# Kernel optimization log

Hardware: AMD Instinct MI355X
Metric: run time of the kernel (lower is better)

The kernel has to match this reference:

```python
import jax, jax.numpy as jnp
import numpy as np

N_NODES = 100000
N_EDGES = 3200000
BN_EPS = 1e-5


def setup_inputs() -> dict:
    key = jax.random.key(0)
    ks = jax.random.split(key, 16)
    return {
        "x": jax.random.normal(ks[0], (N_NODES, 2), jnp.float32),
        "eq_labels": jax.random.randint(ks[1], (N_NODES,), 0, 32, jnp.int32),
        "edge_index": jax.random.randint(ks[2], (2, N_EDGES), 0, N_NODES, jnp.int32),
        "eq_emb": jax.random.normal(ks[3], (32, 8), jnp.float32),
        "W1_0": jax.random.normal(ks[4], (10, 64), jnp.float32) * 0.3,
        "b1_0": jnp.zeros((64,), jnp.float32),
        "W2_0": jax.random.normal(ks[5], (64, 64), jnp.float32) * 0.12,
        "b2_0": jnp.zeros((64,), jnp.float32),
        "eps_0": jnp.zeros((), jnp.float32),
        "gamma_0": jnp.ones((64,), jnp.float32),
        "beta_0": jnp.zeros((64,), jnp.float32),
        "W1_s": jax.random.normal(ks[6], (2, 64, 64), jnp.float32) * 0.12,
        "b1_s": jnp.zeros((2, 64), jnp.float32),
        "W2_s": jax.random.normal(ks[7], (2, 64, 64), jnp.float32) * 0.12,
        "b2_s": jnp.zeros((2, 64), jnp.float32),
        "eps_s": jnp.zeros((2,), jnp.float32),
        "gamma_s": jnp.ones((2, 64), jnp.float32),
        "beta_s": jnp.zeros((2, 64), jnp.float32),
        "Wf": jax.random.normal(ks[8], (64, 1), jnp.float32) * 0.12,
        "bf": jnp.zeros((1,), jnp.float32),
    }


def _gin_bn_relu(h, src, dst, W1, b1, W2, b2, eps, gamma, beta):
    # GINConv: (1+eps)*x_i + sum_{j->i} x_j, then 2-layer ReLU MLP, then BN, ReLU
    agg = jax.ops.segment_sum(h[src], dst, num_segments=N_NODES)
    h = (1.0 + eps) * h + agg
    h = jax.nn.relu(h @ W1 + b1)
    h = jax.nn.relu(h @ W2 + b2)
    mu = jnp.mean(h, axis=0)
    var = jnp.var(h, axis=0)
    h = (h - mu) * jax.lax.rsqrt(var + BN_EPS) * gamma + beta
    return jax.nn.relu(h)


def reference(x, eq_labels, edge_index, eq_emb, W1_0, b1_0, W2_0, b2_0, eps_0,
              gamma_0, beta_0, W1_s, b1_s, W2_s, b2_s, eps_s, gamma_s, beta_s,
              Wf, bf):
    src, dst = edge_index[0], edge_index[1]
    h = jnp.concatenate([x, eq_emb[eq_labels]], axis=-1)  # [N, 10]
    h = _gin_bn_relu(h, src, dst, W1_0, b1_0, W2_0, b2_0, eps_0, gamma_0, beta_0)
    for i in range(2):
        h = _gin_bn_relu(h, src, dst, W1_s[i], b1_s[i], W2_s[i], b2_s[i],
                         eps_s[i], gamma_s[i], beta_s[i])
    return (h @ Wf + bf).squeeze(-1)  # [N]
```

## Files before the change

kernel.cpp:

```cpp
#include <hip/hip_runtime.h>

#define N_NODES 100000
#define N_EDGES 3200000
#define BN_EPS 1e-5f

#define BLK_NODES 128
#define NBLK 782
#define CHUNK 16384
#define NW ((N_EDGES + CHUNK - 1) / CHUNK)
#define BCAP 4480
#define CUR_PAD 16
#define NSLICE 32

typedef unsigned int uint;
typedef unsigned short ushort;
typedef _Float16 half_t;
typedef __attribute__((ext_vector_type(8))) _Float16 h8v;
typedef __attribute__((ext_vector_type(4))) float f4v;

__device__ inline float bf_lo(uint u) { return __uint_as_float(u << 16); }
__device__ inline float bf_hi(uint u) { return __uint_as_float(u & 0xffff0000u); }
__device__ inline float h_lo(uint u) {
    union { ushort s; half_t h; } r; r.s = (ushort)(u & 0xffffu); return (float)r.h;
}
__device__ inline float h_hi(uint u) {
    union { ushort s; half_t h; } r; r.s = (ushort)(u >> 16); return (float)r.h;
}
__device__ inline ushort f2bf(float a) {
    uint ua = __float_as_uint(a); ua += 0x7fffu + ((ua >> 16) & 1u);
    return (ushort)(ua >> 16);
}
__device__ inline ushort f2h(float a) {
    union { half_t h; ushort u; } r;
    r.h = (half_t)a;
    return r.u;
}
__device__ inline uint packh2(float a, float b) {
    return (uint)f2h(a) | ((uint)f2h(b) << 16);
}
__device__ inline h8v loadH(const ushort* p) {
    union { uint4 q; h8v f; } r;
    r.q = *(const uint4*)p;
    return r.f;
}
__device__ inline h8v loadHh(const half_t* p) {
    union { uint4 q; h8v f; } r;
    r.q = *(const uint4*)p;
    return r.f;
}
__device__ inline f4v mfma16(h8v a, h8v b, f4v c) {
    return __builtin_amdgcn_mfma_f32_16x16x32_f16(a, b, c, 0, 0, 0);
}

__global__ __launch_bounds__(256) void k_h0(const float* __restrict__ x,
                                            const int* __restrict__ lab,
                                            const float* __restrict__ emb,
                                            ushort* __restrict__ h0,
                                            const float* __restrict__ W1_0,
                                            const float* __restrict__ W2_0,
                                            const float* __restrict__ W1_s,
                                            const float* __restrict__ W2_s,
                                            ushort* __restrict__ W0t,
                                            ushort* __restrict__ W20t,
                                            ushort* __restrict__ Wst, int n) {
    int i = blockIdx.x * blockDim.x + threadIdx.x;
    if (i < n) {
        float v[16];
        v[0] = x[2 * i];
        v[1] = x[2 * i + 1];
        int L = lab[i];
#pragma unroll
        for (int k = 0; k < 8; k++) v[2 + k] = emb[L * 8 + k];
#pragma unroll
        for (int k = 10; k < 16; k++) v[k] = 0.f;
        uint o8[8];
#pragma unroll
        for (int k = 0; k < 8; k++) o8[k] = packh2(v[2 * k], v[2 * k + 1]);
        uint4* o = (uint4*)(h0 + (size_t)i * 16);
        o[0] = uint4{o8[0], o8[1], o8[2], o8[3]};
        o[1] = uint4{o8[4], o8[5], o8[6], o8[7]};
    }
    if (blockIdx.x == 0) {
        int t = threadIdx.x;
        for (int j = t; j < 64 * 32; j += 256) {
            int nn = j >> 5, k = j & 31;
            W0t[j] = (k < 10) ? f2h(W1_0[k * 64 + nn]) : (ushort)0;
        }
        for (int j = t; j < 4096; j += 256) {
            int nn = j >> 6, k = j & 63;
            W20t[j] = f2h(W2_0[k * 64 + nn]);
        }
        for (int l = 0; l < 2; l++) {
            const float* w1 = W1_s + l * 4096;
            const float* w2 = W2_s + l * 4096;
            for (int j = t; j < 4096; j += 256) {
                int nn = j >> 6, k = j & 63;
                Wst[l * 8192 + j] = f2h(w1[k * 64 + nn]);
                Wst[l * 8192 + 4096 + j] = f2h(w2[k * 64 + nn]);
            }
        }
    }
}

__global__ __launch_bounds__(256) void k_fill(const int* __restrict__ src,
                                              const int* __restrict__ dst,
                                              int* __restrict__ gcur,
                                              int* __restrict__ bucket) {
    __shared__ int cnt[NBLK];
    __shared__ int off[NBLK];
    int t = threadIdx.x;
    for (int b = t; b < NBLK; b += 256) cnt[b] = 0;
    __syncthreads();
    int my0 = blockIdx.x * CHUNK + t * 64;
    for (int k = 0; k < 64; k += 4) {
        int e = my0 + k;
        if (e + 3 < N_EDGES) {
            int4 d4 = *(const int4*)(dst + e);
            atomicAdd(&cnt[d4.x >> 7], 1);
            atomicAdd(&cnt[d4.y >> 7], 1);
            atomicAdd(&cnt[d4.z >> 7], 1);
            atomicAdd(&cnt[d4.w >> 7], 1);
        } else {
#pragma unroll
            for (int kk = 0; kk < 4; kk++) {
                int ee = e + kk;
                if (ee < N_EDGES) atomicAdd(&cnt[dst[ee] >> 7], 1);
            }
        }
    }
    __syncthreads();
    for (int b = t; b < NBLK; b += 256) {
        int c = cnt[b];
        off[b] = (c > 0) ? atomicAdd(&gcur[b * CUR_PAD], c) : 0;
    }
    __syncthreads();
    for (int k = 0; k < 64; k += 4) {
        int e = my0 + k;
        if (e + 3 < N_EDGES) {
            int4 d4 = *(const int4*)(dst + e);
            int4 s4 = *(const int4*)(src + e);
            int dd[4] = {d4.x, d4.y, d4.z, d4.w};
            int ss[4] = {s4.x, s4.y, s4.z, s4.w};
#pragma unroll
            for (int kk = 0; kk < 4; kk++) {
                int b = dd[kk] >> 7;
                int p = atomicAdd(&off[b], 1);
                if (p < BCAP)
                    bucket[(size_t)b * BCAP + p] = ((dd[kk] & 127) << 17) | ss[kk];
            }
        } else {
#pragma unroll
            for (int kk = 0; kk < 4; kk++) {
                int ee = e + kk;
                if (ee < N_EDGES) {
                    int d = dst[ee], s = src[ee];
                    int b = d >> 7;
                    int p = atomicAdd(&off[b], 1);
                    if (p < BCAP)
                        bucket[(size_t)b * BCAP + p] = ((d & 127) << 17) | s;
                }
            }
        }
    }
}

__global__ __launch_bounds__(256) void k_sort(const int* __restrict__ gcur,
                                              const int* __restrict__ bucket,
                                              int* __restrict__ col2,
                                              int2* __restrict__ nodeoff, int n) {
    __shared__ int cnt[BLK_NODES];
    __shared__ int scn[BLK_NODES];
    __shared__ int cur[BLK_NODES];
    int t = threadIdx.x;
    int blk = blockIdx.x;
    if (t < BLK_NODES) cnt[t] = 0;
    __syncthreads();
    int cc = min(gcur[blk * CUR_PAD], BCAP);
    const int* bb = bucket + (size_t)blk * BCAP;
    for (int i = t; i < cc; i += 256) atomicAdd(&cnt[bb[i] >> 17], 1);
    __syncthreads();
    if (t < BLK_NODES) scn[t] = cnt[t];
    __syncthreads();
#pragma unroll
    for (int off = 1; off < BLK_NODES; off <<= 1) {
        int v = (t >= off && t < BLK_NODES) ? scn[t - off] : 0;
        __syncthreads();
        if (t < BLK_NODES) scn[t] += v;
        __syncthreads();
    }
    if (t < BLK_NODES) {
        int start = scn[t] - cnt[t];
        cur[t] = start;
        int node = blk * BLK_NODES + t;
        if (node < n) nodeoff[node] = int2{blk * BCAP + start, cnt[t]};
    }
    __syncthreads();
    int* out = col2 + (size_t)blk * BCAP;
    for (int i = t; i < cc; i += 256) {
        int w = bb[i];
        int p = atomicAdd(&cur[w >> 17], 1);
        out[p] = w & 0x1FFFF;
    }
}

__global__ __launch_bounds__(256, 4) void k_layer0M(const ushort* __restrict__ h0,
                                                    const int2* __restrict__ nodeoff,
                                                    const int* __restrict__ col,
                                                    const float* __restrict__ epsp,
                                                    const ushort* __restrict__ W0t,
                                                    const float* __restrict__ b1,
                                                    const ushort* __restrict__ W20t,
                                                    const float* __restrict__ b2,
                                                    ushort* __restrict__ hraw,
                                                    float* __restrict__ part_out) {
    __shared__ half_t buf[4][16][72];
    int t = threadIdx.x, w = t >> 6, lane = t & 63;
    int base = blockIdx.x * 64 + w * 16;
    float ep = 1.f + *epsp;
    int hl = lane >> 5, l5 = lane & 31;
    int q = l5 & 3, g = l5 >> 2;
    const uint* hb = (const uint*)h0;

    int nj = base + (lane & 15);
    int2 no2 = nodeoff[nj];
    int myStart = no2.x;
    int myDeg = (nj < N_NODES) ? no2.y : 0;

    int stC, dgC, mxC, wvC, wv2C;
    {
        stC = __shfl(myStart, hl, 64);
        dgC = __shfl(myDeg, hl, 64);
        int dA = __shfl(myDeg, 0, 64), dB = __shfl(myDeg, 1, 64);
        mxC = max(dA, dB);
        wvC = (dgC > 0) ? col[stC + min(l5, dgC - 1)] : 0;
        wv2C = (mxC > 32) ? ((dgC > 32) ? col[stC + min(32 + l5, dgC - 1)] : wvC) : 0;
    }

    for (int r = 0; r < 8; r++) {
        int stN = 0, dgN = 0, mxN = 0, wvN = 0, wv2N = 0;
        if (r < 7) {
            stN = __shfl(myStart, 2 * (r + 1) + hl, 64);
            dgN = __shfl(myDeg, 2 * (r + 1) + hl, 64);
            int dA = __shfl(myDeg, 2 * (r + 1), 64);
            int dB = __shfl(myDeg, 2 * (r + 1) + 1, 64);
            mxN = max(dA, dB);
            wvN = (dgN > 0) ? col[stN + min(l5, dgN - 1)] : 0;
            wv2N = (mxN > 32) ? ((dgN > 32) ? col[stN + min(32 + l5, dgN - 1)] : wvN) : 0;
        }
        int deg = dgC, mx = mxC;
        float ac[4] = {0.f, 0.f, 0.f, 0.f};
        if (mx > 0) {
            int idx[4];
#pragma unroll
            for (int i = 0; i < 4; i++) idx[i] = __shfl(wvC, (hl << 5) + g + 8 * i, 64);
            uint2 rows[4];
#pragma unroll
            for (int i = 0; i < 4; i++)
                rows[i] = *(const uint2*)(hb + (size_t)idx[i] * 8 + q * 2);
#pragma unroll
            for (int i = 0; i < 4; i++) {
                float m = (g + 8 * i < deg) ? 1.f : 0.f;
                ac[0] = fmaf(m, h_lo(rows[i].x), ac[0]);
                ac[1] = fmaf(m, h_hi(rows[i].x), ac[1]);
                ac[2] = fmaf(m, h_lo(rows[i].y), ac[2]);
                ac[3] = fmaf(m, h_hi(rows[i].y), ac[3]);
            }
            if (mx > 32) {
                int idx2[4];
#pragma unroll
                for (int i = 0; i < 4; i++) idx2[i] = __shfl(wv2C, (hl << 5) + g + 8 * i, 64);
                uint2 rows2[4];
#pragma unroll
                for (int i = 0; i < 4; i++)
                    rows2[i] = *(const uint2*)(hb + (size_t)idx2[i] * 8 + q * 2);
#pragma unroll
                for (int i = 0; i < 4; i++) {
                    float m = (32 + g + 8 * i < deg) ? 1.f : 0.f;
                    ac[0] = fmaf(m, h_lo(rows2[i].x), ac[0]);
                    ac[1] = fmaf(m, h_hi(rows2[i].x), ac[1]);
                    ac[2] = fmaf(m, h_lo(rows2[i].y), ac[2]);
                    ac[3] = fmaf(m, h_hi(rows2[i].y), ac[3]);
                }
                for (int e = 64 + g; e < deg; e += 8) {
                    uint2 v = *(const uint2*)(hb + (size_t)col[stC + e] * 8 + q * 2);
                    ac[0] += h_lo(v.x); ac[1] += h_hi(v.x);
                    ac[2] += h_lo(v.y); ac[3] += h_hi(v.y);
                }
            }
        }
#pragma unroll
        for (int o = 4; o < 32; o <<= 1) {
#pragma unroll
            for (int k = 0; k < 4; k++) ac[k] += __shfl_xor(ac[k], o, 64);
        }
        int node = base + 2 * r + hl;
        bool valid = node < N_NODES;
        int nodeC = valid ? node : 0;
        float vm = valid ? ep : 0.f;
        uint2 sv = *(const uint2*)(hb + (size_t)nodeC * 8 + q * 2);
        ac[0] = fmaf(vm, h_lo(sv.x), ac[0]);
        ac[1] = fmaf(vm, h_hi(sv.x), ac[1]);
        ac[2] = fmaf(vm, h_lo(sv.y), ac[2]);
        ac[3] = fmaf(vm, h_hi(sv.y), ac[3]);
        if (!valid) { ac[0] = ac[1] = ac[2] = ac[3] = 0.f; }
        if (g == 0) {
            int nl = 2 * r + hl;
            *(uint2*)&buf[w][nl][q * 4] = uint2{packh2(ac[0], ac[1]), packh2(ac[2], ac[3])};
            *(uint2*)&buf[w][nl][16 + q * 4] = uint2{0u, 0u};
        }
        stC = stN; dgC = dgN; mxC = mxN; wvC = wvN; wv2C = wv2N;
    }
    int mr = lane & 15, kq = lane >> 4, nc = lane & 15;
    h8v A0 = loadHh(&buf[w][mr][kq * 8]);
#pragma unroll
    for (int nt = 0; nt < 4; nt++) {
        float bb = b1[nt * 16 + nc];
        f4v c = {bb, bb, bb, bb};
        c = mfma16(A0, loadH(W0t + (nt * 16 + nc) * 32 + kq * 8), c);
#pragma unroll
        for (int r2 = 0; r2 < 4; r2++)
            buf[w][kq * 4 + r2][nt * 16 + nc] = (half_t)fmaxf(c[r2], 0.f);
    }
    h8v P0 = loadHh(&buf[w][mr][kq * 8]);
    h8v P1 = loadHh(&buf[w][mr][32 + kq * 8]);
    float sA[4], sB[4];
#pragma unroll
    for (int nt = 0; nt < 4; nt++) { sA[nt] = 0.f; sB[nt] = 0.f; }
#pragma unroll
    for (int nt = 0; nt < 4; nt++) {
        float bb = b2[nt * 16 + nc];
        f4v c = {bb, bb, bb, bb};
        c = mfma16(P0, loadH(W20t + (nt * 16 + nc) * 64 + kq * 8), c);
        c = mfma16(P1, loadH(W20t + (nt * 16 + nc) * 64 + 32 + kq * 8), c);
#pragma unroll
        for (int r2 = 0; r2 < 4; r2++) {
            int node = base + kq * 4 + r2;
            float vv = fmaxf(c[r2], 0.f);
            if (node < N_NODES) {
                sA[nt] += vv;
                sB[nt] = fmaf(vv, vv, sB[nt]);
                hraw[(size_t)node * 64 + nt * 16 + nc] = f2h(vv);
            }
        }
    }
#pragma unroll
    for (int o = 16; o < 64; o <<= 1) {
#pragma unroll
        for (int nt = 0; nt < 4; nt++) {
            sA[nt] += __shfl_xor(sA[nt], o, 64);
            sB[nt] += __shfl_xor(sB[nt], o, 64);
        }
    }
    if (kq == 0) {
        float* pp = part_out + (blockIdx.x & (NSLICE - 1)) * 128;
#pragma unroll
        for (int nt = 0; nt < 4; nt++) {
            atomicAdd(&pp[nt * 16 + nc], sA[nt]);
            atomicAdd(&pp[64 + nt * 16 + nc], sB[nt]);
        }
    }
}

__global__ __launch_bounds__(256) void k_act(const ushort* __restrict__ hraw,
                                             const float* __restrict__ part,
                                             const float* __restrict__ gamma,
                                             const float* __restrict__ beta,
                                             ushort* __restrict__ act, float invn) {
    __shared__ float st[128];
    __shared__ float sc[64], sh[64];
    int t = threadIdx.x;
    if (t < 128) {
        float S = 0.f;
#pragma unroll 8
        for (int s = 0; s < NSLICE; s++) S += part[s * 128 + t];
        st[t] = S;
    }
    __syncthreads();
    if (t < 64) {
        float mu = st[t] * invn;
        float var = fmaxf(st[64 + t] * invn - mu * mu, 0.f);
        float s = gamma[t] * rsqrtf(var + BN_EPS);
        sc[t] = s;
        sh[t] = beta[t] - mu * s;
    }
    __syncthreads();
    int base = (blockIdx.x * 256 + t) * 4;
    int f0 = base & 63;
    uint2 hv = *(const uint2*)(hraw + base);
    float a0 = fmaxf(fmaf(h_lo(hv.x), sc[f0 + 0], sh[f0 + 0]), 0.f);
    float a1 = fmaxf(fmaf(h_hi(hv.x), sc[f0 + 1], sh[f0 + 1]), 0.f);
    float a2 = fmaxf(fmaf(h_lo(hv.y), sc[f0 + 2], sh[f0 + 2]), 0.f);
    float a3 = fmaxf(fmaf(h_hi(hv.y), sc[f0 + 3], sh[f0 + 3]), 0.f);
    uint2 o;
    o.x = (uint)f2bf(a0) | ((uint)f2bf(a1) << 16);
    o.y = (uint)f2bf(a2) | ((uint)f2bf(a3) << 16);
    *(uint2*)(act + base) = o;
}

__global__ __launch_bounds__(256, 4) void k_layerM(const uint* __restrict__ actin,
                                                   const int2* __restrict__ nodeoff,
                                                   const int* __restrict__ col,
                                                   const float* __restrict__ epsp,
                                                   const ushort* __restrict__ W1t,
                                                   const float* __restrict__ b1,
                                                   const ushort* __restrict__ W2t,
                                                   const float* __restrict__ b2,
                                                   ushort* __restrict__ hraw,
                                                   float* __restrict__ part_out) {
    __shared__ half_t buf[4][16][72];
    int t = threadIdx.x, w = t >> 6, lane = t & 63;
    int base = blockIdx.x * 64 + w * 16;
    float ep = 1.f + *epsp;
    int hl = lane >> 5, l5 = lane & 31;
    int q = l5 & 7, g = l5 >> 3;
    const uint4* hb4 = (const uint4*)actin;

    int nj = base + (lane & 15);
    int2 no2 = nodeoff[nj];
    int myStart = no2.x;
    int myDeg = (nj < N_NODES) ? no2.y : 0;

    int stC, dgC, mxC, wvC, wv2C;
    {
        stC = __shfl(myStart, hl, 64);
        dgC = __shfl(myDeg, hl, 64);
        int dA = __shfl(myDeg, 0, 64), dB = __shfl(myDeg, 1, 64);
        mxC = max(dA, dB);
        wvC = (dgC > 0) ? col[stC + min(l5, dgC - 1)] : 0;
        wv2C = (mxC > 32) ? ((dgC > 32) ? col[stC + min(32 + l5, dgC - 1)] : wvC) : 0;
    }

    for (int r = 0; r < 8; r++) {
        int stN = 0, dgN = 0, mxN = 0, wvN = 0, wv2N = 0;
        if (r < 7) {
            stN = __shfl(myStart, 2 * (r + 1) + hl, 64);
            dgN = __shfl(myDeg, 2 * (r + 1) + hl, 64);
            int dA = __shfl(myDeg, 2 * (r + 1), 64);
            int dB = __shfl(myDeg, 2 * (r + 1) + 1, 64);
            mxN = max(dA, dB);
            wvN = (dgN > 0) ? col[stN + min(l5, dgN - 1)] : 0;
            wv2N = (mxN > 32) ? ((dgN > 32) ? col[stN + min(32 + l5, dgN - 1)] : wvN) : 0;
        }
        int deg = dgC, mx = mxC;
        float acc[8];
#pragma unroll
        for (int k = 0; k < 8; k++) acc[k] = 0.f;
        auto procm = [&](uint4 v, float m) {
            acc[0] = fmaf(m, bf_lo(v.x), acc[0]);
            acc[1] = fmaf(m, bf_hi(v.x), acc[1]);
            acc[2] = fmaf(m, bf_lo(v.y), acc[2]);
            acc[3] = fmaf(m, bf_hi(v.y), acc[3]);
            acc[4] = fmaf(m, bf_lo(v.z), acc[4]);
            acc[5] = fmaf(m, bf_hi(v.z), acc[5]);
            acc[6] = fmaf(m, bf_lo(v.w), acc[6]);
            acc[7] = fmaf(m, bf_hi(v.w), acc[7]);
        };
        if (mx > 0) {
            int idx[8];
#pragma unroll
            for (int i = 0; i < 8; i++) idx[i] = __shfl(wvC, (hl << 5) + g + 4 * i, 64);
            uint4 rows[8];
#pragma unroll
            for (int i = 0; i < 8; i++) rows[i] = hb4[(size_t)idx[i] * 8 + q];
#pragma unroll
            for (int i = 0; i < 8; i++) procm(rows[i], (g + 4 * i < deg) ? 1.f : 0.f);
            if (mx > 32) {
                int idx2[8];
#pragma unroll
                for (int i = 0; i < 8; i++) idx2[i] = __shfl(wv2C, (hl << 5) + g + 4 * i, 64);
                uint4 rows2[8];
#pragma unroll
                for (int i = 0; i < 8; i++) rows2[i] = hb4[(size_t)idx2[i] * 8 + q];
#pragma unroll
                for (int i = 0; i < 8; i++) procm(rows2[i], (32 + g + 4 * i < deg) ? 1.f : 0.f);
                for (int e = 64 + g; e < deg; e += 4)
                    procm(hb4[(size_t)col[stC + e] * 8 + q], 1.f);
            }
        }
#pragma unroll
        for (int o = 8; o < 32; o <<= 1) {
#pragma unroll
            for (int k = 0; k < 8; k++) acc[k] += __shfl_xor(acc[k], o, 64);
        }
        int node = base + 2 * r + hl;
        bool valid = node < N_NODES;
        int nodeC = valid ? node : 0;
        float vm = valid ? ep : 0.f;
        uint4 v = hb4[(size_t)nodeC * 8 + q];
        acc[0] = fmaf(vm, bf_lo(v.x), acc[0]);
        acc[1] = fmaf(vm, bf_hi(v.x), acc[1]);
        acc[2] = fmaf(vm, bf_lo(v.y), acc[2]);
        acc[3] = fmaf(vm, bf_hi(v.y), acc[3]);
        acc[4] = fmaf(vm, bf_lo(v.z), acc[4]);
        acc[5] = fmaf(vm, bf_hi(v.z), acc[5]);
        acc[6] = fmaf(vm, bf_lo(v.w), acc[6]);
        acc[7] = fmaf(vm, bf_hi(v.w), acc[7]);
        if (!valid) {
#pragma unroll
            for (int k = 0; k < 8; k++) acc[k] = 0.f;
        }
        if (g == 0) {
            int nl = 2 * r + hl;
            *(uint2*)&buf[w][nl][q * 8 + 0] = uint2{packh2(acc[0], acc[1]), packh2(acc[2], acc[3])};
            *(uint2*)&buf[w][nl][q * 8 + 4] = uint2{packh2(acc[4], acc[5]), packh2(acc[6], acc[7])};
        }
        stC = stN; dgC = dgN; mxC = mxN; wvC = wvN; wv2C = wv2N;
    }
    int mr = lane & 15, kq = lane >> 4, nc = lane & 15;
    h8v A0 = loadHh(&buf[w][mr][kq * 8]);
    h8v A1 = loadHh(&buf[w][mr][32 + kq * 8]);
#pragma unroll
    for (int nt = 0; nt < 4; nt++) {
        float bb = b1[nt * 16 + nc];
        f4v c = {bb, bb, bb, bb};
        c = mfma16(A0, loadH(W1t + (nt * 16 + nc) * 64 + kq * 8), c);
        c = mfma16(A1, loadH(W1t + (nt * 16 + nc) * 64 + 32 + kq * 8), c);
#pragma unroll
        for (int r2 = 0; r2 < 4; r2++)
            buf[w][kq * 4 + r2][nt * 16 + nc] = (half_t)fmaxf(c[r2], 0.f);
    }
    h8v P0 = loadHh(&buf[w][mr][kq * 8]);
    h8v P1 = loadHh(&buf[w][mr][32 + kq * 8]);
    float sA[4], sB[4];
#pragma unroll
    for (int nt = 0; nt < 4; nt++) { sA[nt] = 0.f; sB[nt] = 0.f; }
#pragma unroll
    for (int nt = 0; nt < 4; nt++) {
        float bb = b2[nt * 16 + nc];
        f4v c = {bb, bb, bb, bb};
        c = mfma16(P0, loadH(W2t + (nt * 16 + nc) * 64 + kq * 8), c);
        c = mfma16(P1, loadH(W2t + (nt * 16 + nc) * 64 + 32 + kq * 8), c);
#pragma unroll
        for (int r2 = 0; r2 < 4; r2++) {
            int node = base + kq * 4 + r2;
            float vv = fmaxf(c[r2], 0.f);
            if (node < N_NODES) {
                sA[nt] += vv;
                sB[nt] = fmaf(vv, vv, sB[nt]);
                hraw[(size_t)node * 64 + nt * 16 + nc] = f2h(vv);
            }
        }
    }
#pragma unroll
    for (int o = 16; o < 64; o <<= 1) {
#pragma unroll
        for (int nt = 0; nt < 4; nt++) {
            sA[nt] += __shfl_xor(sA[nt], o, 64);
            sB[nt] += __shfl_xor(sB[nt], o, 64);
        }
    }
    if (kq == 0) {
        float* pp = part_out + (blockIdx.x & (NSLICE - 1)) * 128;
#pragma unroll
        for (int nt = 0; nt < 4; nt++) {
            atomicAdd(&pp[nt * 16 + nc], sA[nt]);
            atomicAdd(&pp[64 + nt * 16 + nc], sB[nt]);
        }
    }
}

__global__ __launch_bounds__(256) void k_out(const ushort* __restrict__ hraw,
                                             const float* __restrict__ part,
                                             const float* __restrict__ gamma,
                                             const float* __restrict__ beta,
                                             const float* __restrict__ Wf,
                                             const float* __restrict__ bfp,
                                             float* __restrict__ out, int n,
                                             float invn) {
    __shared__ float st[128];
    __shared__ float sc[64], sh[64];
    int t = threadIdx.x;
    if (t < 128) {
        float S = 0.f;
#pragma unroll 8
        for (int s = 0; s < NSLICE; s++) S += part[s * 128 + t];
        st[t] = S;
    }
    __syncthreads();
    if (t < 64) {
        float mu = st[t] * invn;
        float var = fmaxf(st[64 + t] * invn - mu * mu, 0.f);
        float s = gamma[t] * rsqrtf(var + BN_EPS);
        sc[t] = s;
        sh[t] = beta[t] - mu * s;
    }
    __syncthreads();
    int i = blockIdx.x * blockDim.x + threadIdx.x;
    if (i >= n) return;
    float acc = *bfp;
    const uint2* h2 = (const uint2*)(hraw + (size_t)i * 64);
#pragma unroll
    for (int qq = 0; qq < 16; qq++) {
        uint2 v = h2[qq];
        int j = qq * 4;
        acc = fmaf(fmaxf(fmaf(h_lo(v.x), sc[j + 0], sh[j + 0]), 0.f), Wf[j + 0], acc);
        acc = fmaf(fmaxf(fmaf(h_hi(v.x), sc[j + 1], sh[j + 1]), 0.f), Wf[j + 1], acc);
        acc = fmaf(fmaxf(fmaf(h_lo(v.y), sc[j + 2], sh[j + 2]), 0.f), Wf[j + 2], acc);
        acc = fmaf(fmaxf(fmaf(h_hi(v.y), sc[j + 3], sh[j + 3]), 0.f), Wf[j + 3], acc);
    }
    out[i] = acc;
}

extern "C" void kernel_launch(void* const* d_in, const int* in_sizes, int n_in,
                              void* d_out, int out_size, void* d_ws, size_t ws_size,
                              hipStream_t stream) {
    const float* x      = (const float*)d_in[0];
    const int*   lab    = (const int*)d_in[1];
    const int*   edge   = (const int*)d_in[2];
    const float* emb    = (const float*)d_in[3];
    const float* W1_0   = (const float*)d_in[4];
    const float* b1_0   = (const float*)d_in[5];
    const float* W2_0   = (const float*)d_in[6];
    const float* b2_0   = (const float*)d_in[7];
    const float* eps_0  = (const float*)d_in[8];
    const float* gamma_0= (const float*)d_in[9];
    const float* beta_0 = (const float*)d_in[10];
    const float* W1_s   = (const float*)d_in[11];
    const float* b1_s   = (const float*)d_in[12];
    const float* W2_s   = (const float*)d_in[13];
    const float* b2_s   = (const float*)d_in[14];
    const float* eps_s  = (const float*)d_in[15];
    const float* gamma_s= (const float*)d_in[16];
    const float* beta_s = (const float*)d_in[17];
    const float* Wf     = (const float*)d_in[18];
    const float* bf     = (const float*)d_in[19];

    const int N = N_NODES, E = N_EDGES;
    const int* srcp = edge;
    const int* dstp = edge + E;

    char* p = (char*)d_ws;
    auto alloc = [&](size_t bytes) {
        void* r = (void*)p;
        p += (bytes + 255) & ~(size_t)255;
        return r;
    };
    int* bucket  = (int*)alloc((size_t)NBLK * BCAP * 4);
    int* col2    = (int*)alloc((size_t)NBLK * BCAP * 4);
    int* gcur    = (int*)alloc((size_t)NBLK * CUR_PAD * 4);
    int* nodeoff = (int*)alloc((size_t)(N + 64) * 8);
    ushort* hraw = (ushort*)alloc((size_t)N * 64 * 2);
    ushort* act  = (ushort*)alloc((size_t)N * 64 * 2);
    ushort* h0   = (ushort*)alloc((size_t)N * 16 * 2);
    float* parts = (float*)alloc(3 * NSLICE * 128 * 4);
    ushort* W0t  = (ushort*)alloc(64 * 32 * 2);
    ushort* W20t = (ushort*)alloc(4096 * 2);
    ushort* Wst  = (ushort*)alloc(2 * 8192 * 2);

    hipMemsetAsync(gcur, 0, (size_t)NBLK * CUR_PAD * 4, stream);
    hipMemsetAsync(parts, 0, 3 * NSLICE * 128 * 4, stream);

    const int TB = 256;
    const int gN = (N + TB - 1) / TB;
    const int gM = (N + 63) / 64;
    const int gA = N * 64 / 1024;
    const float invn = 1.0f / (float)N;

    k_h0<<<gN, TB, 0, stream>>>(x, lab, emb, h0, W1_0, W2_0, W1_s, W2_s,
                                W0t, W20t, Wst, N);
    k_fill<<<NW, TB, 0, stream>>>(srcp, dstp, gcur, bucket);
    k_sort<<<NBLK, TB, 0, stream>>>(gcur, bucket, col2, (int2*)nodeoff, N);

    k_layer0M<<<gM, TB, 0, stream>>>(h0, (const int2*)nodeoff, col2, eps_0, W0t,
                                     b1_0, W20t, b2_0, hraw,
                                     parts + 0 * NSLICE * 128);
    k_act<<<gA, TB, 0, stream>>>(hraw, parts + 0 * NSLICE * 128, gamma_0, beta_0,
                                 act, invn);

    k_layerM<<<gM, TB, 0, stream>>>((const uint*)act, (const int2*)nodeoff, col2,
                                    eps_s + 0, Wst + 0 * 8192, b1_s + 0 * 64,
                                    Wst + 0 * 8192 + 4096, b2_s + 0 * 64,
                                    hraw, parts + 1 * NSLICE * 128);
    k_act<<<gA, TB, 0, stream>>>(hraw, parts + 1 * NSLICE * 128, gamma_s + 0 * 64,
                                 beta_s + 0 * 64, act, invn);

    k_layerM<<<gM, TB, 0, stream>>>((const uint*)act, (const int2*)nodeoff, col2,
                                    eps_s + 1, Wst + 1 * 8192, b1_s + 1 * 64,
                                    Wst + 1 * 8192 + 4096, b2_s + 1 * 64,
                                    hraw, parts + 2 * NSLICE * 128);

    k_out<<<gN, TB, 0, stream>>>(hraw, parts + 2 * NSLICE * 128,
                                 gamma_s + 1 * 64, beta_s + 1 * 64, Wf, bf,
                                 (float*)d_out, N, invn);
}
```

Baseline: 385.1 us.

## Software-pipeline neighbor gathers two rounds ahead in GIN aggregation kernels

Restructures the per-wave neighbor aggregation loop so column indices are fetched two rounds ahead and the first 32 neighbor rows for the next node pair are loaded while the current pair is accumulated. It also removes the degree-based branches around the first two 32-edge gathers, so both batches are always loaded and masked. The aim is to hide gather latency behind arithmetic. In exchange it raises register pressure and issues unconditional loads for low-degree nodes.

```diff
diff --git a/kernel.cpp b/kernel.cpp
--- a/kernel.cpp
+++ b/kernel.cpp
@@ -51,6 +51,20 @@
 __device__ inline f4v mfma16(h8v a, h8v b, f4v c) {
     return __builtin_amdgcn_mfma_f32_16x16x32_f16(a, b, c, 0, 0, 0);
 }
+
+#define FETCH_COLS(rr, st, dg, mx, wv, wv2)                                   \
+    {                                                                         \
+        int _r = (rr);                                                        \
+        st = __shfl(myStart, 2 * _r + hl, 64);                                \
+        dg = __shfl(myDeg, 2 * _r + hl, 64);                                  \
+        int _dA = __shfl(myDeg, 2 * _r, 64);                                  \
+        int _dB = __shfl(myDeg, 2 * _r + 1, 64);                              \
+        mx = max(_dA, _dB);                                                   \
+        int _e1 = min(l5, dg - 1); _e1 = _e1 < 0 ? 0 : _e1;                   \
+        int _e2 = min(32 + l5, dg - 1); _e2 = _e2 < 0 ? 0 : _e2;              \
+        wv = col[st + _e1];                                                   \
+        wv2 = col[st + _e2];                                                  \
+    }
 
 __global__ __launch_bounds__(256) void k_h0(const float* __restrict__ x,
                                             const int* __restrict__ lab,
@@ -223,69 +237,59 @@
 
     int nj = base + (lane & 15);
     int2 no2 = nodeoff[nj];
-    int myStart = no2.x;
-    int myDeg = (nj < N_NODES) ? no2.y : 0;
+    bool njv = nj < N_NODES;
+    int myStart = njv ? no2.x : 0;
+    int myDeg = njv ? no2.y : 0;
 
     int stC, dgC, mxC, wvC, wv2C;
-    {
-        stC = __shfl(myStart, hl, 64);
-        dgC = __shfl(myDeg, hl, 64);
-        int dA = __shfl(myDeg, 0, 64), dB = __shfl(myDeg, 1, 64);
-        mxC = max(dA, dB);
-        wvC = (dgC > 0) ? col[stC + min(l5, dgC - 1)] : 0;
-        wv2C = (mxC > 32) ? ((dgC > 32) ? col[stC + min(32 + l5, dgC - 1)] : wvC) : 0;
+    int stN, dgN, mxN, wvN, wv2N;
+    FETCH_COLS(0, stC, dgC, mxC, wvC, wv2C);
+    FETCH_COLS(1, stN, dgN, mxN, wvN, wv2N);
+    uint2 rowsC[4];
+#pragma unroll
+    for (int i = 0; i < 4; i++) {
+        int ix = __shfl(wvC, (hl << 5) + g + 8 * i, 64);
+        rowsC[i] = *(const uint2*)(hb + (size_t)ix * 8 + q * 2);
     }
 
     for (int r = 0; r < 8; r++) {
-        int stN = 0, dgN = 0, mxN = 0, wvN = 0, wv2N = 0;
-        if (r < 7) {
-            stN = __shfl(myStart, 2 * (r + 1) + hl, 64);
-            dgN = __shfl(myDeg, 2 * (r + 1) + hl, 64);
-            int dA = __shfl(myDeg, 2 * (r + 1), 64);
-            int dB = __shfl(myDeg, 2 * (r + 1) + 1, 64);
-            mxN = max(dA, dB);
-            wvN = (dgN > 0) ? col[stN + min(l5, dgN - 1)] : 0;
-            wv2N = (mxN > 32) ? ((dgN > 32) ? col[stN + min(32 + l5, dgN - 1)] : wvN) : 0;
-        }
-        int deg = dgC, mx = mxC;
+        int stNN, dgNN, mxNN, wvNN, wv2NN;
+        FETCH_COLS(min(r + 2, 7), stNN, dgNN, mxNN, wvNN, wv2NN);
+        uint2 rows2[4];
+#pragma unroll
+        for (int i = 0; i < 4; i++) {
+            int ix = __shfl(wv2C, (hl << 5) + g + 8 * i, 64);
+            rows2[i] = *(const uint2*)(hb + (size_t)ix * 8 + q * 2);
+        }
+        int deg = dgC;
         float ac[4] = {0.f, 0.f, 0.f, 0.f};
-        if (mx > 0) {
-            int idx[4];
-#pragma unroll
-            for (int i = 0; i < 4; i++) idx[i] = __shfl(wvC, (hl << 5) + g + 8 * i, 64);
-            uint2 rows[4];
-#pragma unroll
-            for (int i = 0; i < 4; i++)
-                rows[i] = *(const uint2*)(hb + (size_t)idx[i] * 8 + q * 2);
-#pragma unroll
-            for (int i = 0; i < 4; i++) {
-                float m = (g + 8 * i < deg) ? 1.f : 0.f;
-                ac[0] = fmaf(m, h_lo(rows[i].x), ac[0]);
-                ac[1] = fmaf(m, h_hi(rows[i].x), ac[1]);
-                ac[2] = fmaf(m, h_lo(rows[i].y), ac[2]);
-                ac[3] = fmaf(m, h_hi(rows[i].y), ac[3]);
-            }
-            if (mx > 32) {
-                int idx2[4];
-#pragma unroll
-                for (int i = 0; i < 4; i++) idx2[i] = __shfl(wv2C, (hl << 5) + g + 8 * i, 64);
-                uint2 rows2[4];
-#pragma unroll
-                for (int i = 0; i < 4; i++)
-                    rows2[i] = *(const uint2*)(hb + (size_t)idx2[i] * 8 + q * 2);
-#pragma unroll
-                for (int i = 0; i < 4; i++) {
-                    float m = (32 + g + 8 * i < deg) ? 1.f : 0.f;
-                    ac[0] = fmaf(m, h_lo(rows2[i].x), ac[0]);
-                    ac[1] = fmaf(m, h_hi(rows2[i].x), ac[1]);
-                    ac[2] = fmaf(m, h_lo(rows2[i].y), ac[2]);
-                    ac[3] = fmaf(m, h_hi(rows2[i].y), ac[3]);
-                }
-                for (int e = 64 + g; e < deg; e += 8) {
-                    uint2 v = *(const uint2*)(hb + (size_t)col[stC + e] * 8 + q * 2);
-                    ac[0] += h_lo(v.x); ac[1] += h_hi(v.x);
-                    ac[2] += h_lo(v.y); ac[3] += h_hi(v.y);
-                }
+#pragma unroll
+        for (int i = 0; i < 4; i++) {
+            float m = (g + 8 * i < deg) ? 1.f : 0.f;
+            ac[0] = fmaf(m, h_lo(rowsC[i].x), ac[0]);
+            ac[1] = fmaf(m, h_hi(rowsC[i].x), ac[1]);
+            ac[2] = fmaf(m, h_lo(rowsC[i].y), ac[2]);
+            ac[3] = fmaf(m, h_hi(rowsC[i].y), ac[3]);
+        }
+        uint2 rowsN[4];
+#pragma unroll
+        for (int i = 0; i < 4; i++) {
+            int ix = __shfl(wvN, (hl << 5) + g + 8 * i, 64);
+            rowsN[i] = *(const uint2*)(hb + (size_t)ix * 8 + q * 2);
+        }
+#pragma unroll
+        for (int i = 0; i < 4; i++) {
+            float m = (32 + g + 8 * i < deg) ? 1.f : 0.f;
+            ac[0] = fmaf(m, h_lo(rows2[i].x), ac[0]);
+            ac[1] = fmaf(m, h_hi(rows2[i].x), ac[1]);
+            ac[2] = fmaf(m, h_lo(rows2[i].y), ac[2]);
+            ac[3] = fmaf(m, h_hi(rows2[i].y), ac[3]);
+        }
+        if (mxC > 64) {
+            for (int e = 64 + g; e < deg; e += 8) {
+                uint2 v = *(const uint2*)(hb + (size_t)col[stC + e] * 8 + q * 2);
+                ac[0] += h_lo(v.x); ac[1] += h_hi(v.x);
+                ac[2] += h_lo(v.y); ac[3] += h_hi(v.y);
             }
         }
 #pragma unroll
@@ -309,6 +313,9 @@
             *(uint2*)&buf[w][nl][16 + q * 4] = uint2{0u, 0u};
         }
         stC = stN; dgC = dgN; mxC = mxN; wvC = wvN; wv2C = wv2N;
+        stN = stNN; dgN = dgNN; mxN = mxNN; wvN = wvNN; wv2N = wv2NN;
+#pragma unroll
+        for (int i = 0; i < 4; i++) rowsC[i] = rowsN[i];
     }
     int mr = lane & 15, kq = lane >> 4, nc = lane & 15;
     h8v A0 = loadHh(&buf[w][mr][kq * 8]);
@@ -417,31 +424,31 @@
 
     int nj = base + (lane & 15);
     int2 no2 = nodeoff[nj];
-    int myStart = no2.x;
-    int myDeg = (nj < N_NODES) ? no2.y : 0;
+    bool njv = nj < N_NODES;
+    int myStart = njv ? no2.x : 0;
+    int myDeg = njv ? no2.y : 0;
 
     int stC, dgC, mxC, wvC, wv2C;
-    {
-        stC = __shfl(myStart, hl, 64);
-        dgC = __shfl(myDeg, hl, 64);
-        int dA = __shfl(myDeg, 0, 64), dB = __shfl(myDeg, 1, 64);
-        mxC = max(dA, dB);
-        wvC = (dgC > 0) ? col[stC + min(l5, dgC - 1)] : 0;
-        wv2C = (mxC > 32) ? ((dgC > 32) ? col[stC + min(32 + l5, dgC - 1)] : wvC) : 0;
+    int stN, dgN, mxN, wvN, wv2N;
+    FETCH_COLS(0, stC, dgC, mxC, wvC, wv2C);
+    FETCH_COLS(1, stN, dgN, mxN, wvN, wv2N);
+    uint4 rowsC[8];
+#pragma unroll
+    for (int i = 0; i < 8; i++) {
+        int ix = __shfl(wvC, (hl << 5) + g + 4 * i, 64);
+        rowsC[i] = hb4[(size_t)ix * 8 + q];
     }
 
     for (int r = 0; r < 8; r++) {
-        int stN = 0, dgN = 0, mxN = 0, wvN = 0, wv2N = 0;
-        if (r < 7) {
-            stN = __shfl(myStart, 2 * (r + 1) + hl, 64);
-            dgN = __shfl(myDeg, 2 * (r + 1) + hl, 64);
-            int dA = __shfl(myDeg, 2 * (r + 1), 64);
-            int dB = __shfl(myDeg, 2 * (r + 1) + 1, 64);
-            mxN = max(dA, dB);
-            wvN = (dgN > 0) ? col[stN + min(l5, dgN - 1)] : 0;
-            wv2N = (mxN > 32) ? ((dgN > 32) ? col[stN + min(32 + l5, dgN - 1)] : wvN) : 0;
-        }
-        int deg = dgC, mx = mxC;
+        int stNN, dgNN, mxNN, wvNN, wv2NN;
+        FETCH_COLS(min(r + 2, 7), stNN, dgNN, mxNN, wvNN, wv2NN);
+        uint4 rows2[8];
+#pragma unroll
+        for (int i = 0; i < 8; i++) {
+            int ix = __shfl(wv2C, (hl << 5) + g + 4 * i, 64);
+            rows2[i] = hb4[(size_t)ix * 8 + q];
+        }
+        int deg = dgC;
         float acc[8];
 #pragma unroll
         for (int k = 0; k < 8; k++) acc[k] = 0.f;
@@ -455,27 +462,19 @@
             acc[6] = fmaf(m, bf_lo(v.w), acc[6]);
             acc[7] = fmaf(m, bf_hi(v.w), acc[7]);
         };
-        if (mx > 0) {
-            int idx[8];
-#pragma unroll
-            for (int i = 0; i < 8; i++) idx[i] = __shfl(wvC, (hl << 5) + g + 4 * i, 64);
-            uint4 rows[8];
-#pragma unroll
-            for (int i = 0; i < 8; i++) rows[i] = hb4[(size_t)idx[i] * 8 + q];
-#pragma unroll
-            for (int i = 0; i < 8; i++) procm(rows[i], (g + 4 * i < deg) ? 1.f : 0.f);
-            if (mx > 32) {
-                int idx2[8];
-#pragma unroll
-                for (int i = 0; i < 8; i++) idx2[i] = __shfl(wv2C, (hl << 5) + g + 4 * i, 64);
-                uint4 rows2[8];
-#pragma unroll
-                for (int i = 0; i < 8; i++) rows2[i] = hb4[(size_t)idx2[i] * 8 + q];
-#pragma unroll
-                for (int i = 0; i < 8; i++) procm(rows2[i], (32 + g + 4 * i < deg) ? 1.f : 0.f);
-                for (int e = 64 + g; e < deg; e += 4)
-                    procm(hb4[(size_t)col[stC + e] * 8 + q], 1.f);
-            }
+#pragma unroll
+        for (int i = 0; i < 8; i++) procm(rowsC[i], (g + 4 * i < deg) ? 1.f : 0.f);
+        uint4 rowsN[8];
+#pragma unroll
+        for (int i = 0; i < 8; i++) {
+            int ix = __shfl(wvN, (hl << 5) + g + 4 * i, 64);
+            rowsN[i] = hb4[(size_t)ix * 8 + q];
+        }
+#pragma unroll
+        for (int i = 0; i < 8; i++) procm(rows2[i], (32 + g + 4 * i < deg) ? 1.f : 0.f);
+        if (mxC > 64) {
+            for (int e = 64 + g; e < deg; e += 4)
+                procm(hb4[(size_t)col[stC + e] * 8 + q], 1.f);
         }
 #pragma unroll
         for (int o = 8; o < 32; o <<= 1) {
@@ -505,6 +504,9 @@
             *(uint2*)&buf[w][nl][q * 8 + 4] = uint2{packh2(acc[4], acc[5]), packh2(acc[6], acc[7])};
         }
         stC = stN; dgC = dgN; mxC = mxN; wvC = wvN; wv2C = wv2N;
+        stN = stNN; dgN = dgNN; mxN = mxNN; wvN = wvNN; wv2N = wv2NN;
+#pragma unroll
+        for (int i = 0; i < 8; i++) rowsC[i] = rowsN[i];
     }
     int mr = lane & 15, kq = lane >> 4, nc = lane & 15;
     h8v A0 = loadHh(&buf[w][mr][kq * 8]);
```

After: 384.7 us. No clear change (-0.1%).
